# Performance work log

Hardware: AMD Instinct MI355X
Metric: run time of the kernel (lower is better)

## Reference

```python
import jax, jax.numpy as jnp
import numpy as np

T, H = 4096, 2048


def setup_inputs() -> dict:
    key = jax.random.key(0)
    k_a, k_b, k_x = jax.random.split(key, 3)
    # glorot-style init matching the module: uniform(-1,1) * sqrt(2/sum(shape))
    a = jax.random.uniform(k_a, (H,), minval=-1.0, maxval=1.0) * jnp.sqrt(2.0 / H)
    B = jax.random.uniform(k_b, (H, H), minval=-1.0, maxval=1.0) * jnp.sqrt(2.0 / (2 * H))
    x = jax.random.normal(k_x, (T, H), dtype=jnp.float32)
    return {"x": x, "a": a, "B": B}


def reference(x, a, B):
    # x: (T, H); per-timestep s_t = B.T @ x_t  ->  s = x @ B, laid out NCH = (1, H, T)
    Tl, Hl = x.shape
    s = jnp.einsum("th,hk->kt", x, B)[None]  # (1, H, T)
    # depthwise causal kernel: k[h, t] = a[h]**t, time as final dim, flipped for conv
    exponents = jnp.arange(Tl)
    kernel = jnp.power(a[:, None], exponents)          # (H, T)
    kernel_flipped = jnp.flip(kernel, axis=-1)[:, None, :]  # (H, 1, T) OIH
    s_padded = jnp.pad(s, ((0, 0), (0, 0), (Tl - 1, 0)))    # causal left-pad
    conv_out = jax.lax.conv_general_dilated(
        s_padded, kernel_flipped,
        window_strides=(1,), padding="VALID",
        dimension_numbers=("NCH", "OIH", "NCH"),
        feature_group_count=Hl,
    )  # (1, H, T): h_t[h] = sum_{k<=t} a[h]**(t-k) * s_k[h]
    return jnp.transpose(conv_out, (0, 2, 1))  # (1, T, H)
```

## Files before the change

### kernel.cpp

```cpp
#include <hip/hip_runtime.h>
#include <stdint.h>

#define TDIM 4096
#define HDIM 2048

#define BM 128
#define BN 128
#define BK 64
#define NKT (HDIM / BK)
#define AREG  18432
#define PERBUF 34816
#define SSTR   132

typedef short short8 __attribute__((ext_vector_type(8)));
typedef float f32x4 __attribute__((ext_vector_type(4)));

__device__ __forceinline__ uint16_t f2bf(float f) {
  uint32_t u = __builtin_bit_cast(uint32_t, f);
  u += 0x7fffu + ((u >> 16) & 1u);
  return (uint16_t)(u >> 16);
}
__device__ __forceinline__ float bf2f(uint32_t h) {
  uint32_t u = h << 16;
  return __builtin_bit_cast(float, u);
}

__device__ __forceinline__ void async_copy16(const void* gsrc, void* ldst) {
  __builtin_amdgcn_global_load_lds(
      (const __attribute__((address_space(1))) uint32_t*)gsrc,
      (__attribute__((address_space(3))) uint32_t*)ldst,
      16, 0, 0);
}

__global__ void prep(const float* __restrict__ x, const float* __restrict__ B,
                     uint16_t* __restrict__ xb, uint16_t* __restrict__ Bt) {
  __shared__ uint16_t tile[64][68];
  const int t = threadIdx.x;
  if (blockIdx.x < 4096) {
    size_t i = ((size_t)blockIdx.x * 256 + t) * 8;
    float4 v0 = *(const float4*)(x + i);
    float4 v1 = *(const float4*)(x + i + 4);
    union { uint16_t h[8]; uint4 v; } o;
    o.h[0] = f2bf(v0.x); o.h[1] = f2bf(v0.y); o.h[2] = f2bf(v0.z); o.h[3] = f2bf(v0.w);
    o.h[4] = f2bf(v1.x); o.h[5] = f2bf(v1.y); o.h[6] = f2bf(v1.z); o.h[7] = f2bf(v1.w);
    *(uint4*)(xb + i) = o.v;
  } else {
    const int bid = blockIdx.x - 4096;
    const int n0 = (bid & 31) * 64;
    const int k0 = (bid >> 5) * 64;
    {
      const int r  = t >> 4;
      const int c4 = (t & 15) * 4;
#pragma unroll
      for (int i = 0; i < 4; ++i) {
        int rr = r + i * 16;
        float4 v = *(const float4*)&B[(size_t)(k0 + rr) * HDIM + n0 + c4];
        union { uint16_t h[4]; uint2 u; } o;
        o.h[0] = f2bf(v.x); o.h[1] = f2bf(v.y); o.h[2] = f2bf(v.z); o.h[3] = f2bf(v.w);
        *(uint2*)&tile[rr][c4] = o.u;
      }
    }
    __syncthreads();
    {
      const int nr = t >> 2;
      const int kc = (t & 3) * 4;
#pragma unroll
      for (int i = 0; i < 4; ++i) {
        int kk = kc + i * 16;
        union { uint16_t h[4]; uint2 u; } o;
        o.h[0] = tile[kk][nr];     o.h[1] = tile[kk + 1][nr];
        o.h[2] = tile[kk + 2][nr]; o.h[3] = tile[kk + 3][nr];
        *(uint2*)&Bt[(size_t)(n0 + nr) * HDIM + k0 + kk] = o.u;
      }
    }
  }
}

__global__ __launch_bounds__(512, 4) void gemm_scan(
    const uint16_t* __restrict__ A, const uint16_t* __restrict__ Bt,
    const float* __restrict__ a, float* __restrict__ out) {
  __shared__ __align__(16) char lds[2 * PERBUF];

  const int tid  = threadIdx.x;
  const int lane = tid & 63;
  const int wave = tid >> 6;
  const int wm = (wave >> 2) * 64;
  const int wn = (wave & 3) * 32;
  const int m0 = blockIdx.y * BM;
  const int n0 = blockIdx.x * BN;

  f32x4 acc[4][2] = {};
  f32x4 accw[2] = {};

  const int lr = lane >> 3;
  const int gc = (lane & 7) ^ lr;

  const int fr = lane & 15;
  const int fq = lane >> 4;

  auto issue_tile = [&](int kt2) {
    size_t koff = (size_t)kt2 * (BK * 2);
    char* dst = lds + (kt2 & 1) * PERBUF;
#pragma unroll
    for (int g = wave; g < 18; g += 8) {
      int row = m0 - 16 + g * 8 + lr;
      if (row < 0) row = 0;
      async_copy16((const char*)A + ((size_t)row * HDIM + gc * 8) * 2 + koff,
                   dst + g * 1024);
    }
#pragma unroll
    for (int g = wave; g < 16; g += 8) {
      int row = n0 + g * 8 + lr;
      async_copy16((const char*)Bt + ((size_t)row * HDIM + gc * 8) * 2 + koff,
                   dst + AREG + g * 1024);
    }
  };

  issue_tile(0);
  for (int kt = 0; kt < NKT; ++kt) {
    if (kt + 1 < NKT) {
      issue_tile(kt + 1);
      if (wave < 2) asm volatile("s_waitcnt vmcnt(5)" ::: "memory");
      else          asm volatile("s_waitcnt vmcnt(4)" ::: "memory");
    } else {
      asm volatile("s_waitcnt vmcnt(0)" ::: "memory");
    }
    asm volatile("s_barrier" ::: "memory");

    const char* base = lds + (kt & 1) * PERBUF;
#pragma unroll
    for (int s = 0; s < 2; ++s) {
      short8 af[4], bfr[2], aw;
#pragma unroll
      for (int im = 0; im < 4; ++im) {
        int row = 16 + wm + im * 16 + fr;
        af[im] = *(const short8*)(base + row * 128 + (((s * 4 + fq) ^ (fr & 7)) * 16));
      }
#pragma unroll
      for (int in = 0; in < 2; ++in) {
        int row = wn + in * 16 + fr;
        bfr[in] = *(const short8*)(base + AREG + row * 128 + (((s * 4 + fq) ^ (fr & 7)) * 16));
      }
#pragma unroll
      for (int im = 0; im < 4; ++im)
#pragma unroll
        for (int in = 0; in < 2; ++in)
          acc[im][in] = __builtin_amdgcn_mfma_f32_16x16x32_bf16(
              af[im], bfr[in], acc[im][in], 0, 0, 0);
      if (wave < 4) {
        aw = *(const short8*)(base + fr * 128 + (((s * 4 + fq) ^ (fr & 7)) * 16));
#pragma unroll
        for (int in = 0; in < 2; ++in)
          accw[in] = __builtin_amdgcn_mfma_f32_16x16x32_bf16(
              aw, bfr[in], accw[in], 0, 0, 0);
      }
    }

    asm volatile("s_barrier" ::: "memory");
  }

  uint16_t* Sl = (uint16_t*)lds;
#pragma unroll
  for (int im = 0; im < 4; ++im)
#pragma unroll
    for (int in = 0; in < 2; ++in)
#pragma unroll
      for (int r = 0; r < 4; ++r)
        Sl[(16 + wm + im * 16 + fq * 4 + r) * SSTR + wn + in * 16 + fr] =
            f2bf(acc[im][in][r]);
  if (wave < 4) {
#pragma unroll
    for (int in = 0; in < 2; ++in)
#pragma unroll
      for (int r = 0; r < 4; ++r)
        Sl[(fq * 4 + r) * SSTR + wn + in * 16 + fr] = f2bf(accw[in][r]);
  }
  __syncthreads();

  const int col   = tid & 127;
  const int chunk = tid >> 7;
  const float av  = a[n0 + col];
  float h = 0.f;
  if (!(m0 == 0 && chunk == 0)) {
#pragma unroll
    for (int i = 0; i < 16; ++i)
      h = av * h + bf2f(Sl[(chunk * 32 + i) * SSTR + col]);
  }
  float* op = out + (size_t)(m0 + chunk * 32) * HDIM + n0 + col;
#pragma unroll
  for (int i = 0; i < 32; ++i) {
    h = av * h + bf2f(Sl[(chunk * 32 + 16 + i) * SSTR + col]);
    op[(size_t)i * HDIM] = h;
  }
}

extern "C" void kernel_launch(void* const* d_in, const int* in_sizes, int n_in,
                              void* d_out, int out_size, void* d_ws, size_t ws_size,
                              hipStream_t stream) {
  const float* x = (const float*)d_in[0];
  const float* a = (const float*)d_in[1];
  const float* B = (const float*)d_in[2];
  float* out = (float*)d_out;

  uint16_t* xb  = (uint16_t*)d_ws;
  uint16_t* Btb = (uint16_t*)((char*)d_ws + (size_t)16 * 1024 * 1024);

  prep<<<4096 + 1024, 256, 0, stream>>>(x, B, xb, Btb);
  gemm_scan<<<dim3(HDIM / BN, TDIM / BM), 512, 0, stream>>>(xb, Btb, a, out);
}
```

Baseline: 139.5 us.

## Load B fragments directly from global into registers, shrinking LDS to A-only

The B operand tile is no longer staged through LDS. Each wave loads its own B fragments straight from global memory into registers, one k-tile ahead, and keeps them in a double-buffered register set, so only the A tile stays double-buffered in LDS. The goal is to cut LDS traffic and LDS footprint, which could allow more resident blocks. The cost is more vector registers, redundant global reads of B (the two wave rows each load the same B columns), and retuned waitcnt values that have to match the new count of outstanding loads.

```diff
diff --git a/kernel.cpp b/kernel.cpp
--- a/kernel.cpp
+++ b/kernel.cpp
@@ -8,8 +8,7 @@
 #define BN 128
 #define BK 64
 #define NKT (HDIM / BK)
-#define AREG  18432
-#define PERBUF 34816
+#define APERBUF 18432
 #define SSTR   132
 
 typedef short short8 __attribute__((ext_vector_type(8)));
@@ -79,7 +78,7 @@
 __global__ __launch_bounds__(512, 4) void gemm_scan(
     const uint16_t* __restrict__ A, const uint16_t* __restrict__ Bt,
     const float* __restrict__ a, float* __restrict__ out) {
-  __shared__ __align__(16) char lds[2 * PERBUF];
+  __shared__ __align__(16) char lds[38016];
 
   const int tid  = threadIdx.x;
   const int lane = tid & 63;
@@ -100,63 +99,83 @@
 
   auto issue_tile = [&](int kt2) {
     size_t koff = (size_t)kt2 * (BK * 2);
-    char* dst = lds + (kt2 & 1) * PERBUF;
-#pragma unroll
-    for (int g = wave; g < 18; g += 8) {
-      int row = m0 - 16 + g * 8 + lr;
-      if (row < 0) row = 0;
+    char* dst = lds + (kt2 & 1) * APERBUF;
+    int g = wave;
+    int row = m0 - 16 + g * 8 + lr;
+    if (row < 0) row = 0;
+    async_copy16((const char*)A + ((size_t)row * HDIM + gc * 8) * 2 + koff,
+                 dst + g * 1024);
+    g = wave + 8;
+    row = m0 - 16 + g * 8 + lr;
+    async_copy16((const char*)A + ((size_t)row * HDIM + gc * 8) * 2 + koff,
+                 dst + g * 1024);
+    if (wave < 2) {
+      g = 16 + wave;
+      row = m0 - 16 + g * 8 + lr;
       async_copy16((const char*)A + ((size_t)row * HDIM + gc * 8) * 2 + koff,
                    dst + g * 1024);
     }
-#pragma unroll
-    for (int g = wave; g < 16; g += 8) {
-      int row = n0 + g * 8 + lr;
-      async_copy16((const char*)Bt + ((size_t)row * HDIM + gc * 8) * 2 + koff,
-                   dst + AREG + g * 1024);
-    }
   };
 
+  const char* bp0 = (const char*)Bt + ((size_t)(n0 + wn + fr) * HDIM + fq * 8) * 2;
+  const char* bp1 = bp0 + (size_t)16 * HDIM * 2;
+  short8 bq[2][2], bqn[2][2];
+  auto loadB = [&](int kt2, short8 d[2][2]) {
+#pragma unroll
+    for (int s = 0; s < 2; ++s) {
+      d[s][0] = *(const short8*)(bp0 + (size_t)kt2 * 128 + s * 64);
+      d[s][1] = *(const short8*)(bp1 + (size_t)kt2 * 128 + s * 64);
+    }
+  };
+
   issue_tile(0);
+  asm volatile("" ::: "memory");
+  loadB(0, bq);
+
   for (int kt = 0; kt < NKT; ++kt) {
     if (kt + 1 < NKT) {
       issue_tile(kt + 1);
-      if (wave < 2) asm volatile("s_waitcnt vmcnt(5)" ::: "memory");
-      else          asm volatile("s_waitcnt vmcnt(4)" ::: "memory");
+      asm volatile("" ::: "memory");
+      loadB(kt + 1, bqn);
+      if (wave < 2) asm volatile("s_waitcnt vmcnt(11)" ::: "memory");
+      else          asm volatile("s_waitcnt vmcnt(10)" ::: "memory");
     } else {
-      asm volatile("s_waitcnt vmcnt(0)" ::: "memory");
+      asm volatile("s_waitcnt vmcnt(4)" ::: "memory");
     }
     asm volatile("s_barrier" ::: "memory");
 
-    const char* base = lds + (kt & 1) * PERBUF;
+    const char* base = lds + (kt & 1) * APERBUF;
 #pragma unroll
     for (int s = 0; s < 2; ++s) {
-      short8 af[4], bfr[2], aw;
+      short8 af[4], aw;
 #pragma unroll
       for (int im = 0; im < 4; ++im) {
         int row = 16 + wm + im * 16 + fr;
         af[im] = *(const short8*)(base + row * 128 + (((s * 4 + fq) ^ (fr & 7)) * 16));
       }
 #pragma unroll
-      for (int in = 0; in < 2; ++in) {
-        int row = wn + in * 16 + fr;
-        bfr[in] = *(const short8*)(base + AREG + row * 128 + (((s * 4 + fq) ^ (fr & 7)) * 16));
-      }
-#pragma unroll
       for (int im = 0; im < 4; ++im)
 #pragma unroll
         for (int in = 0; in < 2; ++in)
           acc[im][in] = __builtin_amdgcn_mfma_f32_16x16x32_bf16(
-              af[im], bfr[in], acc[im][in], 0, 0, 0);
+              af[im], bq[s][in], acc[im][in], 0, 0, 0);
       if (wave < 4) {
         aw = *(const short8*)(base + fr * 128 + (((s * 4 + fq) ^ (fr & 7)) * 16));
 #pragma unroll
         for (int in = 0; in < 2; ++in)
           accw[in] = __builtin_amdgcn_mfma_f32_16x16x32_bf16(
-              aw, bfr[in], accw[in], 0, 0, 0);
+              aw, bq[s][in], accw[in], 0, 0, 0);
       }
     }
 
     asm volatile("s_barrier" ::: "memory");
+    if (kt + 1 < NKT) {
+#pragma unroll
+      for (int s = 0; s < 2; ++s)
+#pragma unroll
+        for (int in = 0; in < 2; ++in)
+          bq[s][in] = bqn[s][in];
+    }
   }
 
   uint16_t* Sl = (uint16_t*)lds;
```

New measurement: 172.1 us. +23.3%, slower.
